# Performance work log

Measured on AMD Instinct MI355X. Metric: run time of the kernel, lower is better.

The kernel has to match this reference:

```python
import jax, jax.numpy as jnp
import numpy as np

NEG_SLOPE = 0.2  # PyG GATConv default leaky_relu slope


def gat_conv(x, src, dst, W, a_src, a_dst, b, num_nodes):
    """One PyG-style GATConv layer (concat over heads).
    x: [N, F_in]; src/dst: [E] (message flows src -> dst);
    W: [F_in, H*C]; a_src/a_dst: [H, C]; b: [H*C].
    """
    H, C = a_src.shape
    h = (x @ W).reshape(num_nodes, H, C)              # [N, H, C]
    alpha_src = jnp.sum(h * a_src, axis=-1)           # [N, H]
    alpha_dst = jnp.sum(h * a_dst, axis=-1)           # [N, H]
    e = jax.nn.leaky_relu(alpha_src[src] + alpha_dst[dst], NEG_SLOPE)  # [E, H]
    # segment softmax over incoming edges of each destination node
    m = jax.ops.segment_max(e, dst, num_segments=num_nodes)            # [N, H]
    ex = jnp.exp(e - m[dst])
    s = jax.ops.segment_sum(ex, dst, num_segments=num_nodes)           # [N, H]
    alpha = ex / (s[dst] + 1e-16)                                      # [E, H]
    msg = h[src] * alpha[:, :, None]                                   # [E, H, C]
    out = jax.ops.segment_sum(msg, dst, num_segments=num_nodes)        # [N, H, C]
    return out.reshape(num_nodes, H * C) + b


def setup_inputs() -> dict:
    key = jax.random.key(0)
    ks = jax.random.split(key, 12)
    N, E, F_in, C, H = 50000, 800000, 256, 64, 8
    x = jax.random.normal(ks[0], (N, F_in), dtype=jnp.float32)
    edge_index = jax.random.randint(ks[1], (2, E), 0, N, dtype=jnp.int64)
    glorot = lambda k, shape: jax.random.normal(k, shape, jnp.float32) * np.sqrt(2.0 / (shape[0] + shape[-1]))
    return {
        "x": x,
        "edge_index": edge_index,
        "W1": glorot(ks[2], (F_in, H * C)),
        "att_src1": glorot(ks[3], (H, C)),
        "att_dst1": glorot(ks[4], (H, C)),
        "b1": jnp.zeros((H * C,), jnp.float32),
        "W2": glorot(ks[5], (H * C, 1 * C)),
        "att_src2": glorot(ks[6], (1, C)),
        "att_dst2": glorot(ks[7], (1, C)),
        "b2": jnp.zeros((C,), jnp.float32),
    }


def reference(x, edge_index, W1, att_src1, att_dst1, b1, W2, att_src2, att_dst2, b2):
    N = x.shape[0]
    # add self-loops (PyG GATConv default add_self_loops=True)
    loops = jnp.arange(N, dtype=edge_index.dtype)
    src = jnp.concatenate([edge_index[0], loops])
    dst = jnp.concatenate([edge_index[1], loops])
    h = gat_conv(x, src, dst, W1, att_src1, att_dst1, b1, N)   # [N, 512]
    h = jax.nn.relu(h)                                         # dropout p=0 -> identity
    out = gat_conv(h, src, dst, W2, att_src2, att_dst2, b2, N) # [N, 64]
    return out
```

## Files before the change

### kernel.cpp

```cpp
#include <hip/hip_runtime.h>
#include <hip/hip_bf16.h>
#include <math.h>
#include <type_traits>

#define NEG_SLOPE 0.2f
#define CAP 64

typedef float f32x4 __attribute__((ext_vector_type(4)));
typedef short s16x8 __attribute__((ext_vector_type(8)));
typedef short s16x4 __attribute__((ext_vector_type(4)));

__device__ __forceinline__ float bf2f(ushort s) {
    union { unsigned u; float f; } cv; cv.u = ((unsigned)s) << 16;
    return cv.f;
}
__device__ __forceinline__ ushort f2bf(float f) {
    __hip_bfloat16 b = __float2bfloat16(f);
    union { __hip_bfloat16 b; ushort u; } cv; cv.b = b;
    return cv.u;
}

__device__ __forceinline__ int edge_val(const int* e, long long i, int is64) {
    return is64 ? e[(size_t)(2 * i)] : e[(size_t)i];
}

__global__ void prep_all(const int* __restrict__ e, int* __restrict__ flag,
                         int* __restrict__ counts, int* __restrict__ csr, int N,
                         const float* __restrict__ W1, ushort* __restrict__ W1t, int K1, int N1,
                         const float* __restrict__ W2, ushort* __restrict__ W2t, int K2, int N2) {
    int b = blockIdx.x, tid = threadIdx.x;
    int nbN = (N + 255) >> 8;
    int nbW1 = (K1 * N1 + 255) >> 8;
    if (b < nbN) {
        int i = b * 256 + tid;
        if (i < N) {
            counts[i] = 1;
            csr[(size_t)i * CAP] = i;
        }
    } else if (b == nbN) {
        if (tid < 64) {
            int v = e[2 * tid + 1];
            unsigned long long bl = __ballot(v != 0);
            if (tid == 0) *flag = (bl == 0ull) ? 1 : 0;
        }
    } else if (b < nbN + 1 + nbW1) {
        int idx = (b - nbN - 1) * 256 + tid;
        if (idx < K1 * N1) {
            int k = idx & (K1 - 1), n = idx / K1;
            W1t[(size_t)n * K1 + k] = f2bf(W1[(size_t)k * N1 + n]);
        }
    } else {
        int idx = (b - nbN - 1 - nbW1) * 256 + tid;
        if (idx < K2 * N2) {
            int k = idx & (K2 - 1), n = idx / K2;
            W2t[(size_t)n * K2 + k] = f2bf(W2[(size_t)k * N2 + n]);
        }
    }
}

template <typename AT, typename CT, int BM, int BN, int WR, int WC, int H>
__device__ __forceinline__ void gemm_core(int bx, int by,
                                          const AT* __restrict__ A,
                                          const ushort* __restrict__ Bt,
                                          CT* __restrict__ C,
                                          const float* __restrict__ att_s,
                                          const float* __restrict__ att_d,
                                          float* __restrict__ as_,
                                          float* __restrict__ ad_,
                                          int M, int N, int K) {
    constexpr int BK = 64;
    constexpr int WAVES = WR * WC;
    constexpr int THREADS = WAVES * 64;
    constexpr int MT = BM / WR / 16;
    constexpr int NT = 4;
    static_assert(BN == WC * 64, "each wave-col owns one 64-col head");
    __shared__ __align__(16) ushort As[BM][BK + 8];
    __shared__ __align__(16) ushort Bs[BN][BK + 8];

    int tid = threadIdx.x;
    int wid = tid >> 6, lane = tid & 63;
    int wr = wid / WC, wc = wid % WC;
    int bm = by * BM, bn = bx * BN;
    int l15 = lane & 15, l4 = lane >> 4;

    f32x4 acc[MT][NT] = {};

    for (int k0 = 0; k0 < K; k0 += BK) {
        if constexpr (std::is_same_v<AT, float>) {
#pragma unroll
            for (int p = 0; p < BM * BK / (4 * THREADS); ++p) {
                int idx = p * THREADS + tid;
                int r = idx >> 4;
                int kc = (idx & 15) << 2;
                float4 v = make_float4(0.f, 0.f, 0.f, 0.f);
                if (bm + r < M) v = *(const float4*)&A[(size_t)(bm + r) * K + k0 + kc];
                ushort* dst = &As[r][kc];
                dst[0] = f2bf(v.x); dst[1] = f2bf(v.y);
                dst[2] = f2bf(v.z); dst[3] = f2bf(v.w);
            }
        } else {
#pragma unroll
            for (int p = 0; p < BM * BK / (8 * THREADS); ++p) {
                int idx = p * THREADS + tid;
                int r = idx >> 3;
                int kc = (idx & 7) << 3;
                s16x8 v = {};
                if (bm + r < M) v = *(const s16x8*)&A[(size_t)(bm + r) * K + k0 + kc];
                *(s16x8*)&As[r][kc] = v;
            }
        }
#pragma unroll
        for (int p = 0; p < BN * BK / (8 * THREADS); ++p) {
            int idx = p * THREADS + tid;
            int n = idx >> 3;
            int kc = (idx & 7) << 3;
            s16x8 v = *(const s16x8*)&Bt[(size_t)(bn + n) * K + k0 + kc];
            *(s16x8*)&Bs[n][kc] = v;
        }
        __syncthreads();
#pragma unroll
        for (int kk = 0; kk < BK; kk += 32) {
            s16x8 af[MT], bf[NT];
            int kb = kk + (l4 << 3);
#pragma unroll
            for (int mt = 0; mt < MT; ++mt)
                af[mt] = *(const s16x8*)&As[wr * (BM / WR) + mt * 16 + l15][kb];
#pragma unroll
            for (int nt = 0; nt < NT; ++nt)
                bf[nt] = *(const s16x8*)&Bs[wc * 64 + nt * 16 + l15][kb];
#pragma unroll
            for (int mt = 0; mt < MT; ++mt)
#pragma unroll
                for (int nt = 0; nt < NT; ++nt)
                    acc[mt][nt] = __builtin_amdgcn_mfma_f32_16x16x32_bf16(af[mt], bf[nt], acc[mt][nt], 0, 0, 0);
        }
        __syncthreads();
    }

    int head = (bn >> 6) + wc;
    float asv[NT], adv[NT];
#pragma unroll
    for (int nt = 0; nt < NT; ++nt) {
        asv[nt] = att_s[head * 64 + nt * 16 + l15];
        adv[nt] = att_d[head * 64 + nt * 16 + l15];
    }
#pragma unroll
    for (int mt = 0; mt < MT; ++mt) {
#pragma unroll
        for (int j = 0; j < 4; ++j) {
            int r = bm + wr * (BM / WR) + mt * 16 + (l4 << 2) + j;
            float ps = 0.f, pd = 0.f;
#pragma unroll
            for (int nt = 0; nt < NT; ++nt) {
                float v = acc[mt][nt][j];
                ps += v * asv[nt];
                pd += v * adv[nt];
            }
#pragma unroll
            for (int off = 1; off < 16; off <<= 1) {
                ps += __shfl_xor(ps, off);
                pd += __shfl_xor(pd, off);
            }
            if (r < M) {
                if (l15 == 0) {
                    as_[(size_t)r * H + head] = ps;
                    ad_[(size_t)r * H + head] = pd;
                }
#pragma unroll
                for (int nt = 0; nt < NT; ++nt) {
                    size_t ci = (size_t)r * N + bn + wc * 64 + nt * 16 + l15;
                    if constexpr (std::is_same_v<CT, float>) C[ci] = acc[mt][nt][j];
                    else C[ci] = f2bf(acc[mt][nt][j]);
                }
            }
        }
    }
}

__global__ __launch_bounds__(256) void gemm1_scatter(
        const int* __restrict__ ebuf, int E, int* __restrict__ counts,
        int* __restrict__ csr, const int* __restrict__ flag, int nGemm,
        const float* __restrict__ A, const ushort* __restrict__ Bt,
        ushort* __restrict__ C, const float* __restrict__ att_s,
        const float* __restrict__ att_d, float* __restrict__ as_,
        float* __restrict__ ad_, int M, int N, int K) {
    int g = blockIdx.x;
    if (g < nGemm) {
        int by = (g & 7) + ((g >> 5) << 3);
        int bx = (g >> 3) & 3;
        gemm_core<float, ushort, 128, 128, 2, 2, 8>(bx, by, A, Bt, C,
                                                    att_s, att_d, as_, ad_, M, N, K);
        return;
    }
    int i = (g - nGemm) * 256 + threadIdx.x;
    if (i >= E) return;
    int is64 = *flag;
    int s = edge_val(ebuf, i, is64);
    int d = edge_val(ebuf, (long long)E + i, is64);
    int pos = atomicAdd(&counts[d], 1);
    if (pos < CAP) csr[(size_t)d * CAP + pos] = s;
}

template <typename AT, typename CT, int BM, int BN, int WR, int WC, int H>
__global__ __launch_bounds__(WR * WC * 64) void gemm_mfma(
        const AT* __restrict__ A, const ushort* __restrict__ Bt, CT* __restrict__ C,
        const float* __restrict__ att_s, const float* __restrict__ att_d,
        float* __restrict__ as_, float* __restrict__ ad_, int M, int N, int K) {
    gemm_core<AT, CT, BM, BN, WR, WC, H>(blockIdx.x, blockIdx.y, A, Bt, C,
                                         att_s, att_d, as_, ad_, M, N, K);
}

__global__ __launch_bounds__(256) void gat_fused_l1(
        const ushort* __restrict__ h, const float* __restrict__ as_,
        const float* __restrict__ ad_, const int* __restrict__ counts,
        const int* __restrict__ csr, const float* __restrict__ bias,
        ushort* __restrict__ out1, int N) {
    int n = (blockIdx.x * 256 + threadIdx.x) >> 6;
    if (n >= N) return;
    int l = threadIdx.x & 63;
    size_t base = (size_t)n * CAP;
    int deg = counts[n]; deg = deg > CAP ? CAP : deg;

    int hh = l & 7, e0 = l >> 3;
    float adw = ad_[n * 8 + hh];
    float m = -1e30f, s = 0.f;
    for (int k = e0; k < deg; k += 8) {
        int src = csr[base + k];
        float e = as_[src * 8 + hh] + adw;
        e = e > 0.f ? e : NEG_SLOPE * e;
        float mn = fmaxf(m, e);
        s = s * __expf(m - mn) + __expf(e - mn);
        m = mn;
    }
#pragma unroll
    for (int off = 8; off < 64; off <<= 1) {
        float mo = __shfl_xor(m, off), so = __shfl_xor(s, off);
        float mn = fmaxf(m, mo);
        s = s * __expf(m - mn) + so * __expf(mo - mn);
        m = mn;
    }
    float inv = 1.f / (s + 1e-16f);
    int hd = l >> 3;
    float mh   = __shfl(m, hd);
    float invh = __shfl(inv, hd);
    float adh  = __shfl(adw, hd);

    float acc[8] = {};
    int k = 0;
    for (; k + 4 <= deg; k += 4) {
        int s0 = csr[base + k],     s1 = csr[base + k + 1];
        int s2 = csr[base + k + 2], s3 = csr[base + k + 3];
        s16x8 v0 = *(const s16x8*)&h[((size_t)s0 << 9) + (l << 3)];
        s16x8 v1 = *(const s16x8*)&h[((size_t)s1 << 9) + (l << 3)];
        s16x8 v2 = *(const s16x8*)&h[((size_t)s2 << 9) + (l << 3)];
        s16x8 v3 = *(const s16x8*)&h[((size_t)s3 << 9) + (l << 3)];
        float e0v = as_[s0 * 8 + hd] + adh;
        float e1v = as_[s1 * 8 + hd] + adh;
        float e2v = as_[s2 * 8 + hd] + adh;
        float e3v = as_[s3 * 8 + hd] + adh;
        e0v = e0v > 0.f ? e0v : NEG_SLOPE * e0v;
        e1v = e1v > 0.f ? e1v : NEG_SLOPE * e1v;
        e2v = e2v > 0.f ? e2v : NEG_SLOPE * e2v;
        e3v = e3v > 0.f ? e3v : NEG_SLOPE * e3v;
        float a0 = __expf(e0v - mh);
        float a1 = __expf(e1v - mh);
        float a2 = __expf(e2v - mh);
        float a3 = __expf(e3v - mh);
#pragma unroll
        for (int j = 0; j < 8; ++j)
            acc[j] += a0 * bf2f((ushort)v0[j]) + a1 * bf2f((ushort)v1[j])
                    + a2 * bf2f((ushort)v2[j]) + a3 * bf2f((ushort)v3[j]);
    }
    for (; k < deg; ++k) {
        int s0 = csr[base + k];
        s16x8 v0 = *(const s16x8*)&h[((size_t)s0 << 9) + (l << 3)];
        float e0v = as_[s0 * 8 + hd] + adh;
        e0v = e0v > 0.f ? e0v : NEG_SLOPE * e0v;
        float a0 = __expf(e0v - mh);
#pragma unroll
        for (int j = 0; j < 8; ++j) acc[j] += a0 * bf2f((ushort)v0[j]);
    }
    float4 b0 = *(const float4*)&bias[l * 8];
    float4 b1 = *(const float4*)&bias[l * 8 + 4];
    s16x8 w;
    w[0] = f2bf(fmaxf(acc[0] * invh + b0.x, 0.f));
    w[1] = f2bf(fmaxf(acc[1] * invh + b0.y, 0.f));
    w[2] = f2bf(fmaxf(acc[2] * invh + b0.z, 0.f));
    w[3] = f2bf(fmaxf(acc[3] * invh + b0.w, 0.f));
    w[4] = f2bf(fmaxf(acc[4] * invh + b1.x, 0.f));
    w[5] = f2bf(fmaxf(acc[5] * invh + b1.y, 0.f));
    w[6] = f2bf(fmaxf(acc[6] * invh + b1.z, 0.f));
    w[7] = f2bf(fmaxf(acc[7] * invh + b1.w, 0.f));
    *(s16x8*)&out1[((size_t)n << 9) + (l << 3)] = w;
}

__global__ __launch_bounds__(256) void gat_fused_l2(
        const ushort* __restrict__ h, const float* __restrict__ as_,
        const float* __restrict__ ad_, const int* __restrict__ counts,
        const int* __restrict__ csr, const float* __restrict__ bias,
        float* __restrict__ out, int N) {
    int n = (blockIdx.x * 256 + threadIdx.x) >> 6;
    if (n >= N) return;
    int l = threadIdx.x & 63;
    size_t base = (size_t)n * CAP;
    int deg = counts[n]; deg = deg > CAP ? CAP : deg;
    float adv = ad_[n];

    float m = -1e30f, s = 0.f;
    for (int k = l; k < deg; k += 64) {
        float e = as_[csr[base + k]] + adv;
        e = e > 0.f ? e : NEG_SLOPE * e;
        float mn = fmaxf(m, e);
        s = s * __expf(m - mn) + __expf(e - mn);
        m = mn;
    }
#pragma unroll
    for (int off = 1; off < 64; off <<= 1) {
        float mo = __shfl_xor(m, off), so = __shfl_xor(s, off);
        float mn = fmaxf(m, mo);
        s = s * __expf(m - mn) + so * __expf(mo - mn);
        m = mn;
    }
    float inv = 1.f / (s + 1e-16f);

    int q = l >> 4, c4 = l & 15;
    float a0 = 0.f, a1 = 0.f, a2 = 0.f, a3 = 0.f;
    int k = q;
    for (; k + 12 < deg; k += 16) {
        int sA = csr[base + k],     sB = csr[base + k + 4];
        int sC = csr[base + k + 8], sD = csr[base + k + 12];
        s16x4 vA = *(const s16x4*)&h[((size_t)sA << 6) + (c4 << 2)];
        s16x4 vB = *(const s16x4*)&h[((size_t)sB << 6) + (c4 << 2)];
        s16x4 vC = *(const s16x4*)&h[((size_t)sC << 6) + (c4 << 2)];
        s16x4 vD = *(const s16x4*)&h[((size_t)sD << 6) + (c4 << 2)];
        float eA = as_[sA] + adv, eB = as_[sB] + adv;
        float eC = as_[sC] + adv, eD = as_[sD] + adv;
        eA = eA > 0.f ? eA : NEG_SLOPE * eA;
        eB = eB > 0.f ? eB : NEG_SLOPE * eB;
        eC = eC > 0.f ? eC : NEG_SLOPE * eC;
        eD = eD > 0.f ? eD : NEG_SLOPE * eD;
        float aA = __expf(eA - m), aB = __expf(eB - m);
        float aC = __expf(eC - m), aD = __expf(eD - m);
        a0 += aA * bf2f((ushort)vA[0]) + aB * bf2f((ushort)vB[0])
            + aC * bf2f((ushort)vC[0]) + aD * bf2f((ushort)vD[0]);
        a1 += aA * bf2f((ushort)vA[1]) + aB * bf2f((ushort)vB[1])
            + aC * bf2f((ushort)vC[1]) + aD * bf2f((ushort)vD[1]);
        a2 += aA * bf2f((ushort)vA[2]) + aB * bf2f((ushort)vB[2])
            + aC * bf2f((ushort)vC[2]) + aD * bf2f((ushort)vD[2]);
        a3 += aA * bf2f((ushort)vA[3]) + aB * bf2f((ushort)vB[3])
            + aC * bf2f((ushort)vC[3]) + aD * bf2f((ushort)vD[3]);
    }
    for (; k < deg; k += 4) {
        int sA = csr[base + k];
        s16x4 vA = *(const s16x4*)&h[((size_t)sA << 6) + (c4 << 2)];
        float eA = as_[sA] + adv;
        eA = eA > 0.f ? eA : NEG_SLOPE * eA;
        float aA = __expf(eA - m);
        a0 += aA * bf2f((ushort)vA[0]);
        a1 += aA * bf2f((ushort)vA[1]);
        a2 += aA * bf2f((ushort)vA[2]);
        a3 += aA * bf2f((ushort)vA[3]);
    }
    a0 += __shfl_xor(a0, 16); a0 += __shfl_xor(a0, 32);
    a1 += __shfl_xor(a1, 16); a1 += __shfl_xor(a1, 32);
    a2 += __shfl_xor(a2, 16); a2 += __shfl_xor(a2, 32);
    a3 += __shfl_xor(a3, 16); a3 += __shfl_xor(a3, 32);
    if (q == 0) {
        float4 bv = *(const float4*)&bias[c4 << 2];
        float4 r;
        r.x = a0 * inv + bv.x; r.y = a1 * inv + bv.y;
        r.z = a2 * inv + bv.z; r.w = a3 * inv + bv.w;
        *(float4*)&out[((size_t)n << 6) + (c4 << 2)] = r;
    }
}

extern "C" void kernel_launch(void* const* d_in, const int* in_sizes, int n_in,
                              void* d_out, int out_size, void* d_ws, size_t ws_size,
                              hipStream_t stream) {
    const float* x    = (const float*)d_in[0];
    const int*   ebuf = (const int*)d_in[1];
    const float* W1   = (const float*)d_in[2];
    const float* aS1  = (const float*)d_in[3];
    const float* aD1  = (const float*)d_in[4];
    const float* b1   = (const float*)d_in[5];
    const float* W2   = (const float*)d_in[6];
    const float* aS2  = (const float*)d_in[7];
    const float* aD2  = (const float*)d_in[8];
    const float* b2   = (const float*)d_in[9];
    float* out = (float*)d_out;

    const int F_in = 256, H1 = 8, HC1 = 512, C2 = 64;
    int N = in_sizes[0] / F_in;
    int E = in_sizes[1] / 2;

    char* ws = (char*)d_ws;
    size_t off = 0;
    auto alloc = [&](size_t bytes) -> void* {
        void* p = ws + off;
        off = (off + bytes + 255) & ~(size_t)255;
        return p;
    };
    ushort* h1b    = (ushort*)alloc((size_t)N * HC1 * 2);
    ushort* out1b  = (ushort*)alloc((size_t)N * HC1 * 2);
    float* as1     = (float*)alloc((size_t)N * H1 * 4);
    float* ad1     = (float*)alloc((size_t)N * H1 * 4);
    float* as2     = (float*)alloc((size_t)N * 4);
    float* ad2     = (float*)alloc((size_t)N * 4);
    int*   counts  = (int*)alloc((size_t)N * 4);
    int*   csr     = (int*)alloc((size_t)N * CAP * 4);
    int*   flag    = (int*)alloc(64);
    ushort* W1t    = (ushort*)alloc((size_t)F_in * HC1 * 2);
    ushort* W2t    = (ushort*)alloc((size_t)HC1 * C2 * 2);
    ushort* h2b    = h1b;

    int nbN = (N + 255) >> 8;
    int nbW1 = (F_in * HC1 + 255) >> 8;
    int nbW2 = (HC1 * C2 + 255) >> 8;

    prep_all<<<nbN + 1 + nbW1 + nbW2, 256, 0, stream>>>(
        ebuf, flag, counts, csr, N, W1, W1t, F_in, HC1, W2, W2t, HC1, C2);

    {
        int nby = (N + 127) / 128;
        int nbyPad = (nby + 7) & ~7;
        int nGemm = 4 * nbyPad;
        int nScatter = (E + 255) / 256;
        gemm1_scatter<<<nGemm + nScatter, 256, 0, stream>>>(
            ebuf, E, counts, csr, flag, nGemm,
            x, W1t, h1b, aS1, aD1, as1, ad1, N, HC1, F_in);
    }

    gat_fused_l1<<<(N + 3) / 4, 256, 0, stream>>>(h1b, as1, ad1, counts, csr, b1, out1b, N);

    {
        dim3 g(1, (N + 127) / 128);
        gemm_mfma<ushort, ushort, 128, 64, 4, 1, 1><<<g, 256, 0, stream>>>(
            out1b, W2t, h2b, aS2, aD2, as2, ad2, N, C2, HC1);
    }
    gat_fused_l2<<<(N + 3) / 4, 256, 0, stream>>>(h2b, as2, ad2, counts, csr, b2, out, N);
}
```

Measured before the change: 306.0 us.

## Move self-loop and dtype detection into scatter, memset counts, shrink GEMM2 tile

The count and self-loop initialisation in the prep kernel is replaced by a memset of the counts array. Self-loop edges are now appended inside the scatter blocks, and each scatter block detects the int64 layout itself, so the global flag is gone. The fp32-to-bf16 staging writes to shared memory become one packed 8-byte store instead of four scalar stores. The layer-2 GEMM tile shrinks from 128 to 64 rows to launch more blocks. Self-loops now land at arbitrary CSR positions instead of slot 0, which could change the CAP truncation behaviour.

```diff
diff --git a/kernel.cpp b/kernel.cpp
--- a/kernel.cpp
+++ b/kernel.cpp
@@ -24,33 +24,18 @@
     return is64 ? e[(size_t)(2 * i)] : e[(size_t)i];
 }
 
-__global__ void prep_all(const int* __restrict__ e, int* __restrict__ flag,
-                         int* __restrict__ counts, int* __restrict__ csr, int N,
-                         const float* __restrict__ W1, ushort* __restrict__ W1t, int K1, int N1,
-                         const float* __restrict__ W2, ushort* __restrict__ W2t, int K2, int N2) {
+__global__ void prep_trans(const float* __restrict__ W1, ushort* __restrict__ W1t, int K1, int N1,
+                           const float* __restrict__ W2, ushort* __restrict__ W2t, int K2, int N2) {
     int b = blockIdx.x, tid = threadIdx.x;
-    int nbN = (N + 255) >> 8;
     int nbW1 = (K1 * N1 + 255) >> 8;
-    if (b < nbN) {
-        int i = b * 256 + tid;
-        if (i < N) {
-            counts[i] = 1;
-            csr[(size_t)i * CAP] = i;
-        }
-    } else if (b == nbN) {
-        if (tid < 64) {
-            int v = e[2 * tid + 1];
-            unsigned long long bl = __ballot(v != 0);
-            if (tid == 0) *flag = (bl == 0ull) ? 1 : 0;
-        }
-    } else if (b < nbN + 1 + nbW1) {
-        int idx = (b - nbN - 1) * 256 + tid;
+    if (b < nbW1) {
+        int idx = b * 256 + tid;
         if (idx < K1 * N1) {
             int k = idx & (K1 - 1), n = idx / K1;
             W1t[(size_t)n * K1 + k] = f2bf(W1[(size_t)k * N1 + n]);
         }
     } else {
-        int idx = (b - nbN - 1 - nbW1) * 256 + tid;
+        int idx = (b - nbW1) * 256 + tid;
         if (idx < K2 * N2) {
             int k = idx & (K2 - 1), n = idx / K2;
             W2t[(size_t)n * K2 + k] = f2bf(W2[(size_t)k * N2 + n]);
@@ -94,9 +79,10 @@
                 int kc = (idx & 15) << 2;
                 float4 v = make_float4(0.f, 0.f, 0.f, 0.f);
                 if (bm + r < M) v = *(const float4*)&A[(size_t)(bm + r) * K + k0 + kc];
-                ushort* dst = &As[r][kc];
-                dst[0] = f2bf(v.x); dst[1] = f2bf(v.y);
-                dst[2] = f2bf(v.z); dst[3] = f2bf(v.w);
+                s16x4 pk;
+                pk[0] = (short)f2bf(v.x); pk[1] = (short)f2bf(v.y);
+                pk[2] = (short)f2bf(v.z); pk[3] = (short)f2bf(v.w);
+                *(s16x4*)&As[r][kc] = pk;
             }
         } else {
 #pragma unroll
@@ -178,8 +164,8 @@
 }
 
 __global__ __launch_bounds__(256) void gemm1_scatter(
-        const int* __restrict__ ebuf, int E, int* __restrict__ counts,
-        int* __restrict__ csr, const int* __restrict__ flag, int nGemm,
+        const int* __restrict__ ebuf, int E, int Nn, int* __restrict__ counts,
+        int* __restrict__ csr, int nGemm,
         const float* __restrict__ A, const ushort* __restrict__ Bt,
         ushort* __restrict__ C, const float* __restrict__ att_s,
         const float* __restrict__ att_d, float* __restrict__ as_,
@@ -192,11 +178,23 @@
                                                     att_s, att_d, as_, ad_, M, N, K);
         return;
     }
+    __shared__ int s_is64;
+    if (threadIdx.x < 64) {
+        int v = ebuf[2 * threadIdx.x + 1];
+        unsigned long long bl = __ballot(v != 0);
+        if (threadIdx.x == 0) s_is64 = (bl == 0ull) ? 1 : 0;
+    }
+    __syncthreads();
+    int is64 = s_is64;
     int i = (g - nGemm) * 256 + threadIdx.x;
-    if (i >= E) return;
-    int is64 = *flag;
-    int s = edge_val(ebuf, i, is64);
-    int d = edge_val(ebuf, (long long)E + i, is64);
+    if (i >= E + Nn) return;
+    int s, d;
+    if (i < E) {
+        s = edge_val(ebuf, i, is64);
+        d = edge_val(ebuf, (long long)E + i, is64);
+    } else {
+        s = i - E; d = s;
+    }
     int pos = atomicAdd(&counts[d], 1);
     if (pos < CAP) csr[(size_t)d * CAP + pos] = s;
 }
@@ -408,33 +406,32 @@
     float* ad2     = (float*)alloc((size_t)N * 4);
     int*   counts  = (int*)alloc((size_t)N * 4);
     int*   csr     = (int*)alloc((size_t)N * CAP * 4);
-    int*   flag    = (int*)alloc(64);
     ushort* W1t    = (ushort*)alloc((size_t)F_in * HC1 * 2);
     ushort* W2t    = (ushort*)alloc((size_t)HC1 * C2 * 2);
     ushort* h2b    = h1b;
 
-    int nbN = (N + 255) >> 8;
     int nbW1 = (F_in * HC1 + 255) >> 8;
     int nbW2 = (HC1 * C2 + 255) >> 8;
 
-    prep_all<<<nbN + 1 + nbW1 + nbW2, 256, 0, stream>>>(
-        ebuf, flag, counts, csr, N, W1, W1t, F_in, HC1, W2, W2t, HC1, C2);
+    hipMemsetAsync(counts, 0, (size_t)N * 4, stream);
+
+    prep_trans<<<nbW1 + nbW2, 256, 0, stream>>>(W1, W1t, F_in, HC1, W2, W2t, HC1, C2);
 
     {
         int nby = (N + 127) / 128;
         int nbyPad = (nby + 7) & ~7;
         int nGemm = 4 * nbyPad;
-        int nScatter = (E + 255) / 256;
+        int nScatter = (E + N + 255) / 256;
         gemm1_scatter<<<nGemm + nScatter, 256, 0, stream>>>(
-            ebuf, E, counts, csr, flag, nGemm,
+            ebuf, E, N, counts, csr, nGemm,
             x, W1t, h1b, aS1, aD1, as1, ad1, N, HC1, F_in);
     }
 
     gat_fused_l1<<<(N + 3) / 4, 256, 0, stream>>>(h1b, as1, ad1, counts, csr, b1, out1b, N);
 
     {
-        dim3 g(1, (N + 127) / 128);
-        gemm_mfma<ushort, ushort, 128, 64, 4, 1, 1><<<g, 256, 0, stream>>>(
+        dim3 g(1, (N + 63) / 64);
+        gemm_mfma<ushort, ushort, 64, 64, 4, 1, 1><<<g, 256, 0, stream>>>(
             out1b, W2t, h2b, aS2, aD2, as2, ad2, N, C2, HC1);
     }
     gat_fused_l2<<<(N + 3) / 4, 256, 0, stream>>>(h2b, as2, ad2, counts, csr, b2, out, N);
```

After: 302.7 us. Within noise of the previous version (-1.1%).
